# Performance work log

Hardware: AMD Instinct MI355X
Metric: run time of the kernel (lower is better)

The kernel has to match this reference:

```python
import jax, jax.numpy as jnp
import numpy as np

B, T, D, H = 4, 2048, 1024, 16
DH = D // H  # 64
EPS = 1e-5


def _layernorm(x, g, b):
    mu = jnp.mean(x, axis=-1, keepdims=True)
    var = jnp.var(x, axis=-1, keepdims=True)
    return (x - mu) * jax.lax.rsqrt(var + EPS) * g + b


def setup_inputs() -> dict:
    key = jax.random.key(0)
    ks = jax.random.split(key, 12)
    s = 0.02
    x = jax.random.normal(ks[0], (B, T, D), dtype=jnp.float32)
    # causal mask (the repo registers tril as the eos_mask buffer)
    eos_mask = jnp.broadcast_to(jnp.tril(jnp.ones((T, T), dtype=jnp.int32)), (B, T, T))
    Wq = jax.random.normal(ks[1], (H, D, DH), dtype=jnp.float32) * s
    Wk = jax.random.normal(ks[2], (H, D, DH), dtype=jnp.float32) * s
    Wv = jax.random.normal(ks[3], (H, D, DH), dtype=jnp.float32) * s
    Wp = jax.random.normal(ks[4], (D, D), dtype=jnp.float32) * s
    bp = jnp.zeros((D,), dtype=jnp.float32)
    W1 = jax.random.normal(ks[5], (D, 4 * D), dtype=jnp.float32) * s
    b1 = jnp.zeros((4 * D,), dtype=jnp.float32)
    W2 = jax.random.normal(ks[6], (4 * D, D), dtype=jnp.float32) * s
    b2 = jnp.zeros((D,), dtype=jnp.float32)
    g1 = jnp.ones((D,), dtype=jnp.float32)
    beta1 = jnp.zeros((D,), dtype=jnp.float32)
    g2 = jnp.ones((D,), dtype=jnp.float32)
    beta2 = jnp.zeros((D,), dtype=jnp.float32)
    return dict(x=x, eos_mask=eos_mask, Wq=Wq, Wk=Wk, Wv=Wv, Wp=Wp, bp=bp,
                W1=W1, b1=b1, W2=W2, b2=b2, g1=g1, beta1=beta1, g2=g2, beta2=beta2)


def reference(x, eos_mask, Wq, Wk, Wv, Wp, bp, W1, b1, W2, b2, g1, beta1, g2, beta2):
    # x: [B,T,D]; eos_mask: [B,T,T]
    x1 = _layernorm(x, g1, beta1)
    q = jnp.einsum('btd,hdk->bhtk', x1, Wq)
    k = jnp.einsum('btd,hdk->bhtk', x1, Wk)
    v = jnp.einsum('btd,hdk->bhtk', x1, Wv)
    # NOTE: original scales by 1/sqrt(C) where C = d_model (not d_head)
    scores = jnp.einsum('bhtk,bhsk->bhts', q, k) / np.sqrt(x.shape[-1]).astype(np.float32)
    scores = jnp.where(eos_mask[:, None, :, :] == 0, jnp.float32(-jnp.inf), scores)
    wei = jax.nn.softmax(scores, axis=-1)
    attn = jnp.einsum('bhts,bhsk->bhtk', wei, v)          # [B,H,T,DH]
    attn = attn.transpose(0, 2, 1, 3).reshape(x.shape)    # concat heads -> [B,T,D]
    attn = attn @ Wp + bp
    x2 = x1 + attn
    x3 = _layernorm(x2, g2, beta2)
    mlp = jax.nn.relu(x3 @ W1 + b1) @ W2 + b2
    out = x3 + mlp
    return out
```

## Files before the change

kernel.cpp:

```cpp
#include <hip/hip_runtime.h>


#define B_ 4
#define T_ 2048
#define D_ 1024
#define H_ 16
#define DH_ 64

using u16 = unsigned short;
typedef short bf16x8 __attribute__((ext_vector_type(8)));
typedef float f32x4 __attribute__((ext_vector_type(4)));

#define GLOAD_LDS16(g, l)                                                          \
  __builtin_amdgcn_global_load_lds((const __attribute__((address_space(1))) void*)(g), \
                                   (__attribute__((address_space(3))) void*)(l), 16, 0, 0)

#define CVTPK(d, lo, hi) asm("v_cvt_pk_bf16_f32 %0, %1, %2" : "=v"(d) : "v"(lo), "v"(hi))
#define BARSB() do { __builtin_amdgcn_s_barrier(); __builtin_amdgcn_sched_barrier(0); } while (0)

__device__ __forceinline__ f32x4 mfma16(bf16x8 a, bf16x8 b, f32x4 c) {
  return __builtin_amdgcn_mfma_f32_16x16x32_bf16(a, b, c, 0, 0, 0);
}

__device__ __forceinline__ u16 f2bf(float f) {
  union { float f; unsigned u; } v; v.f = f;
  unsigned r = v.u + 0x7fffu + ((v.u >> 16) & 1u);
  return (u16)(r >> 16);
}
__device__ __forceinline__ float bf2f(u16 h) {
  union { unsigned u; float f; } v; v.u = ((unsigned)h) << 16; return v.f;
}

template<typename TI>
__global__ __launch_bounds__(256)
void ln_kernel(const TI* __restrict__ x, const float* __restrict__ g,
               const float* __restrict__ be, u16* __restrict__ yb)
{
  const int row = blockIdx.x;
  const int tid = threadIdx.x;
  float v0, v1, v2, v3;
  if constexpr (sizeof(TI) == 4) {
    const float4 vx = ((const float4*)(x + (size_t)row * D_))[tid];
    v0 = vx.x; v1 = vx.y; v2 = vx.z; v3 = vx.w;
  } else {
    const ushort4 vx = ((const ushort4*)((const u16*)x + (size_t)row * D_))[tid];
    v0 = bf2f(vx.x); v1 = bf2f(vx.y); v2 = bf2f(vx.z); v3 = bf2f(vx.w);
  }
  float s  = v0 + v1 + v2 + v3;
  float s2 = v0*v0 + v1*v1 + v2*v2 + v3*v3;
#pragma unroll
  for (int m = 1; m < 64; m <<= 1) { s += __shfl_xor(s, m); s2 += __shfl_xor(s2, m); }
  __shared__ float red[8];
  const int w = tid >> 6;
  if ((tid & 63) == 0) { red[w] = s; red[4 + w] = s2; }
  __syncthreads();
  s  = red[0] + red[1] + red[2] + red[3];
  s2 = red[4] + red[5] + red[6] + red[7];
  const float mu   = s * (1.0f / D_);
  const float rstd = rsqrtf(s2 * (1.0f / D_) - mu * mu + 1e-5f);
  const float4 gg = ((const float4*)g)[tid];
  const float4 bb = ((const float4*)be)[tid];
  ushort4 pk;
  pk.x = f2bf((v0 - mu) * rstd * gg.x + bb.x);
  pk.y = f2bf((v1 - mu) * rstd * gg.y + bb.y);
  pk.z = f2bf((v2 - mu) * rstd * gg.z + bb.z);
  pk.w = f2bf((v3 - mu) * rstd * gg.w + bb.w);
  ((ushort4*)(yb + (size_t)row * D_))[tid] = pk;
}

__global__ __launch_bounds__(256)
void transpose_cvt(const float* __restrict__ in, u16* __restrict__ out, int R, int C)
{
  __shared__ float tile[32][33];
  const int c0 = blockIdx.x * 32, r0 = blockIdx.y * 32;
  const float* ip = in + (size_t)blockIdx.z * R * C;
  u16* op = out + (size_t)blockIdx.z * R * C;
  const int tx = threadIdx.x, ty = threadIdx.y;
#pragma unroll
  for (int j = 0; j < 4; ++j)
    tile[ty + j * 8][tx] = ip[(size_t)(r0 + ty + j * 8) * C + (c0 + tx)];
  __syncthreads();
#pragma unroll
  for (int j = 0; j < 4; ++j)
    op[(size_t)(c0 + ty + j * 8) * R + (r0 + tx)] = f2bf(tile[tx][ty + j * 8]);
}

__global__ __launch_bounds__(256)
void transpose_bf(const u16* __restrict__ in, u16* __restrict__ out, int R, int C)
{
  __shared__ u16 tile[32][34];
  const int c0 = blockIdx.x * 32, r0 = blockIdx.y * 32;
  const u16* ip = in + (size_t)blockIdx.z * R * C;
  u16* op = out + (size_t)blockIdx.z * R * C;
  const int tx = threadIdx.x, ty = threadIdx.y;
#pragma unroll
  for (int j = 0; j < 4; ++j)
    tile[ty + j * 8][tx] = ip[(size_t)(r0 + ty + j * 8) * C + (c0 + tx)];
  __syncthreads();
#pragma unroll
  for (int j = 0; j < 4; ++j)
    op[(size_t)(c0 + ty + j * 8) * R + (r0 + tx)] = tile[tx][ty + j * 8];
}

#define MODE_QKV 0
#define MODE_WP 1
#define MODE_MLP1 2
#define MODE_MLP2 3

template<int MODE>
__global__ __launch_bounds__(512, 2)
void gemm256v2(const u16* __restrict__ A, const u16* __restrict__ Bt,
               int M, int N, int K,
               const float* __restrict__ bias, const u16* __restrict__ resid,
               float* __restrict__ outf, u16* __restrict__ outb,
               u16* __restrict__ qo, u16* __restrict__ ko, u16* __restrict__ vo)
{
  __shared__ __align__(16) u16 Ash[2][256 * 64];
  __shared__ __align__(16) u16 Bsh[2][256 * 64];
  const int t = threadIdx.x, w = t >> 6, l = t & 63, lg = l >> 4, lr = l & 15;
  const int wr = w >> 2, wc = w & 3;

  const int gx = gridDim.x;
  const int nwg = gx * gridDim.y;
  const int bid = blockIdx.y * gx + blockIdx.x;
  const int cpx = nwg >> 3;
  const int virt = (bid & 7) * cpx + (bid >> 3);
  const int bn0 = (virt % gx) * 256, bm0 = (virt / gx) * 256;

  f32x4 acc[8][4] = {};

  const int srow = t >> 3;
  const int sc16 = (t & 7) ^ (srow & 7);
  const u16* gAs = A  + (size_t)(bm0 + srow) * K + sc16 * 8;
  const u16* gBs = Bt + (size_t)(bn0 + srow) * K + sc16 * 8;

#define ISS2_A(R, BUF, ko) GLOAD_LDS16(gAs + (size_t)(R) * 64 * K + (ko), &Ash[BUF][(R) * 4096 + w * 512])
#define ISS2_B(R, BUF, ko) GLOAD_LDS16(gBs + (size_t)(R) * 64 * K + (ko), &Bsh[BUF][(R) * 4096 + w * 512])

  const int nkt = K >> 6;
  ISS2_A(0, 0, 0); ISS2_A(1, 0, 0); ISS2_A(2, 0, 0); ISS2_A(3, 0, 0);
  ISS2_B(0, 0, 0); ISS2_B(1, 0, 0); ISS2_B(2, 0, 0); ISS2_B(3, 0, 0);
  if (nkt > 1) {
    ISS2_A(0, 1, 64); ISS2_A(1, 1, 64);
    asm volatile("s_waitcnt vmcnt(2)" ::: "memory");
  } else {
    asm volatile("s_waitcnt vmcnt(0)" ::: "memory");
  }
  BARSB();

  auto rdA = [&](int buf, int m) -> bf16x8 {
    const int r = wr * 128 + m * 16 + lr;
    return *(const bf16x8*)((const char*)&Ash[buf][0] + r * 128 + (((0 + lg) ^ (r & 7)) << 4));
  };
  auto rdA1 = [&](int buf, int m) -> bf16x8 {
    const int r = wr * 128 + m * 16 + lr;
    return *(const bf16x8*)((const char*)&Ash[buf][0] + r * 128 + (((4 + lg) ^ (r & 7)) << 4));
  };
  auto rdB0 = [&](int buf, int n) -> bf16x8 {
    const int r = wc * 64 + n * 16 + lr;
    return *(const bf16x8*)((const char*)&Bsh[buf][0] + r * 128 + (((0 + lg) ^ (r & 7)) << 4));
  };
  auto rdB1 = [&](int buf, int n) -> bf16x8 {
    const int r = wc * 64 + n * 16 + lr;
    return *(const bf16x8*)((const char*)&Bsh[buf][0] + r * 128 + (((4 + lg) ^ (r & 7)) << 4));
  };

  bf16x8 afr[4][2], bfr[4][2];

  for (int i = 0; i < nkt; ++i) {
    const int buf = i & 1, nb = buf ^ 1;
    const size_t k1 = (size_t)(i + 1) << 6, k2 = (size_t)(i + 2) << 6;
    const bool n1 = (i + 1 < nkt), n2 = (i + 2 < nkt);

#pragma unroll
    for (int m = 0; m < 4; ++m) { afr[m][0] = rdA(buf, m); afr[m][1] = rdA1(buf, m); }
#pragma unroll
    for (int n = 0; n < 2; ++n) { bfr[n][0] = rdB0(buf, n); bfr[n][1] = rdB1(buf, n); }
    if (n1) { ISS2_A(2, nb, k1); ISS2_A(3, nb, k1); }
    BARSB();
    __builtin_amdgcn_s_setprio(1);
#pragma unroll
    for (int m = 0; m < 4; ++m)
#pragma unroll
      for (int n = 0; n < 2; ++n) {
        acc[m][n] = mfma16(afr[m][0], bfr[n][0], acc[m][n]);
        acc[m][n] = mfma16(afr[m][1], bfr[n][1], acc[m][n]);
      }
    __builtin_amdgcn_s_setprio(0);
    BARSB();

#pragma unroll
    for (int n = 2; n < 4; ++n) { bfr[n][0] = rdB0(buf, n); bfr[n][1] = rdB1(buf, n); }
    if (n1) { ISS2_B(0, nb, k1); ISS2_B(1, nb, k1); }
    BARSB();
    __builtin_amdgcn_s_setprio(1);
#pragma unroll
    for (int m = 0; m < 4; ++m)
#pragma unroll
      for (int n = 2; n < 4; ++n) {
        acc[m][n] = mfma16(afr[m][0], bfr[n][0], acc[m][n]);
        acc[m][n] = mfma16(afr[m][1], bfr[n][1], acc[m][n]);
      }
    __builtin_amdgcn_s_setprio(0);
    BARSB();

#pragma unroll
    for (int m = 0; m < 4; ++m) { afr[m][0] = rdA(buf, 4 + m); afr[m][1] = rdA1(buf, 4 + m); }
    if (n1) { ISS2_B(2, nb, k1); ISS2_B(3, nb, k1); }
    BARSB();
    __builtin_amdgcn_s_setprio(1);
#pragma unroll
    for (int m = 0; m < 4; ++m)
#pragma unroll
      for (int n = 0; n < 2; ++n) {
        acc[4 + m][n] = mfma16(afr[m][0], bfr[n][0], acc[4 + m][n]);
        acc[4 + m][n] = mfma16(afr[m][1], bfr[n][1], acc[4 + m][n]);
      }
    __builtin_amdgcn_s_setprio(0);
    BARSB();

    if (n2) { ISS2_A(0, buf, k2); ISS2_A(1, buf, k2); }
    BARSB();
    __builtin_amdgcn_s_setprio(1);
#pragma unroll
    for (int m = 0; m < 4; ++m)
#pragma unroll
      for (int n = 2; n < 4; ++n) {
        acc[4 + m][n] = mfma16(afr[m][0], bfr[n][0], acc[4 + m][n]);
        acc[4 + m][n] = mfma16(afr[m][1], bfr[n][1], acc[4 + m][n]);
      }
    __builtin_amdgcn_s_setprio(0);
    if (n2) asm volatile("s_waitcnt vmcnt(2)" ::: "memory");
    else    asm volatile("s_waitcnt vmcnt(0)" ::: "memory");
    BARSB();
  }
#undef ISS2_A
#undef ISS2_B

#pragma unroll
  for (int m = 0; m < 8; ++m) {
#pragma unroll
    for (int n = 0; n < 4; ++n) {
#pragma unroll
      for (int r = 0; r < 4; ++r) {
        const int row = bm0 + wr * 128 + m * 16 + lg * 4 + r;
        const int col = bn0 + wc * 64 + n * 16 + lr;
        float v = acc[m][n][r];
        if constexpr (MODE == MODE_QKV) {
          const int sel = col >> 10, hh = (col >> 6) & 15, dh = col & 63;
          const int bi = row >> 11, tt = row & 2047;
          u16* dst = (sel == 0) ? qo : (sel == 1) ? ko : vo;
          dst[(((size_t)bi * H_ + hh) * T_ + tt) * DH_ + dh] = f2bf(v);
        } else if constexpr (MODE == MODE_MLP1) {
          v += bias[col];
          outb[(size_t)row * N + col] = f2bf(v > 0.f ? v : 0.f);
        }
      }
    }
  }
}

template<int MODE>
__global__ __launch_bounds__(512, 4)
void gemm128(const u16* __restrict__ A, const u16* __restrict__ Bt,
             int M, int N, int K,
             const float* __restrict__ bias, const u16* __restrict__ resid,
             float* __restrict__ outf, u16* __restrict__ outb,
             u16* __restrict__ qo, u16* __restrict__ ko, u16* __restrict__ vo)
{
  __shared__ __align__(16) u16 Ash[2][128 * 64];
  __shared__ __align__(16) u16 Bsh[2][128 * 64];
  const int t = threadIdx.x, w = t >> 6, l = t & 63, lg = l >> 4, lr = l & 15;
  const int wr = w >> 2, wc = w & 3;

  const int gx = gridDim.x;
  const int nwg = gx * gridDim.y;
  const int bid = blockIdx.y * gx + blockIdx.x;
  const int cpx = nwg >> 3;
  const int virt = (bid & 7) * cpx + (bid >> 3);
  const int bn0 = (virt % gx) * 128, bm0 = (virt / gx) * 128;

  f32x4 acc[4][2] = {};

  const int srow = t >> 3;
  const int sc16 = (t & 7) ^ (srow & 7);
  const u16* gAs = A  + (size_t)(bm0 + srow) * K + sc16 * 8;
  const u16* gBs = Bt + (size_t)(bn0 + srow) * K + sc16 * 8;

#define ISS_A(R, BUF, ko) GLOAD_LDS16(gAs + (size_t)(R) * 64 * K + (ko), &Ash[BUF][(R) * 4096 + w * 512])
#define ISS_B(R, BUF, ko) GLOAD_LDS16(gBs + (size_t)(R) * 64 * K + (ko), &Bsh[BUF][(R) * 4096 + w * 512])

  ISS_A(0, 0, 0); ISS_A(1, 0, 0); ISS_B(0, 0, 0); ISS_B(1, 0, 0);
  ISS_A(0, 1, 64); ISS_A(1, 1, 64); ISS_B(0, 1, 64); ISS_B(1, 1, 64);

  auto rdA = [&](int buf, int m, int kk) -> bf16x8 {
    const int r = wr * 64 + m * 16 + lr;
    return *(const bf16x8*)((const char*)&Ash[buf][0] + r * 128 + (((kk * 4 + lg) ^ (r & 7)) << 4));
  };
  auto rdB = [&](int buf, int n, int kk) -> bf16x8 {
    const int r = wc * 32 + n * 16 + lr;
    return *(const bf16x8*)((const char*)&Bsh[buf][0] + r * 128 + (((kk * 4 + lg) ^ (r & 7)) << 4));
  };

  const int nkt = K >> 6;
  for (int i = 0; i < nkt; ++i) {
    const int buf = i & 1;
    if (i + 1 < nkt) asm volatile("s_waitcnt vmcnt(4)" ::: "memory");
    else             asm volatile("s_waitcnt vmcnt(0)" ::: "memory");
    BARSB();

    bf16x8 afr[4][2], bfr[2][2];
#pragma unroll
    for (int m = 0; m < 4; ++m) { afr[m][0] = rdA(buf, m, 0); afr[m][1] = rdA(buf, m, 1); }
#pragma unroll
    for (int n = 0; n < 2; ++n) { bfr[n][0] = rdB(buf, n, 0); bfr[n][1] = rdB(buf, n, 1); }

    __builtin_amdgcn_s_setprio(1);
#pragma unroll
    for (int m = 0; m < 4; ++m)
#pragma unroll
      for (int n = 0; n < 2; ++n) {
        acc[m][n] = mfma16(afr[m][0], bfr[n][0], acc[m][n]);
        acc[m][n] = mfma16(afr[m][1], bfr[n][1], acc[m][n]);
      }
    __builtin_amdgcn_s_setprio(0);
    BARSB();

    if (i + 2 < nkt) {
      const size_t ko = (size_t)(i + 2) << 6;
      ISS_A(0, buf, ko); ISS_A(1, buf, ko); ISS_B(0, buf, ko); ISS_B(1, buf, ko);
    }
  }
#undef ISS_A
#undef ISS_B

#pragma unroll
  for (int m = 0; m < 4; ++m) {
#pragma unroll
    for (int n = 0; n < 2; ++n) {
#pragma unroll
      for (int r = 0; r < 4; ++r) {
        const int row = bm0 + wr * 64 + m * 16 + lg * 4 + r;
        const int col = bn0 + wc * 32 + n * 16 + lr;
        float v = acc[m][n][r];
        if constexpr (MODE == MODE_WP) {
          v += bias[col] + bf2f(resid[(size_t)row * N + col]);
          outb[(size_t)row * N + col] = f2bf(v);
        } else if constexpr (MODE == MODE_MLP2) {
          outf[(size_t)row * N + col] = v + bias[col] + bf2f(resid[(size_t)row * N + col]);
        }
      }
    }
  }
}

__global__ __launch_bounds__(256, 2)
void attn_kernel(const u16* __restrict__ q, const u16* __restrict__ k,
                 const u16* __restrict__ vt, u16* __restrict__ out)
{
  __shared__ __align__(16) u16 Ks[2][4096];
  __shared__ __align__(16) u16 Vs[2][4096];
  const int t = threadIdx.x, w = t >> 6, l = t & 63, lg = l >> 4, lr = l & 15;

  const int bid = blockIdx.x;
  const int virt = (bid & 7) * 256 + (bid >> 3);
  const int bh = (virt >> 8) * 8 + (virt & 7);
  const int qt = 31 - ((virt >> 3) & 31);

  const int b = bh >> 4, h = bh & 15;
  const u16* Qp  = q  + (size_t)bh * T_ * DH_;
  const u16* Kp  = k  + (size_t)bh * T_ * DH_;
  const u16* Vtp = vt + (size_t)bh * T_ * DH_;

  const int qrow = qt * 64 + w * 16 + lr;
  const bf16x8 qf0 = *(const bf16x8*)&Qp[(size_t)qrow * DH_ + lg * 8];
  const bf16x8 qf1 = *(const bf16x8*)&Qp[(size_t)qrow * DH_ + 32 + lg * 8];

  const int srow = t >> 3;
  const int schunk = ((t & 7) ^ (srow & 7)) << 3;
  const u16* Kg = Kp  + (size_t)srow * DH_ + schunk;
  const u16* Vg = Vtp + (size_t)srow * T_  + schunk;

  float m_run = -1e30f, l_run = 0.f;
  f32x4 o[4] = {};
  const float SC2 = 0.03125f * 1.44269504f;
  const float THR2 = 11.5416f;

  GLOAD_LDS16(Kg,            &Ks[0][w * 512]);
  GLOAD_LDS16(Kg + 32 * DH_, &Ks[0][2048 + w * 512]);
  GLOAD_LDS16(Vg,            &Vs[0][w * 512]);
  GLOAD_LDS16(Vg + 32 * T_,  &Vs[0][2048 + w * 512]);
  __syncthreads();

  const int nst = qt + 1;
  for (int st = 0; st < nst; ++st) {
    const int cur = st & 1, nxt = cur ^ 1;
    const bool pf = (st + 1 < nst);
    if (pf) {
      const u16* kg = Kg + (size_t)(st + 1) * 64 * DH_;
      const u16* vg = Vg + (size_t)(st + 1) * 64;
      GLOAD_LDS16(kg,            &Ks[nxt][w * 512]);
      GLOAD_LDS16(kg + 32 * DH_, &Ks[nxt][2048 + w * 512]);
      GLOAD_LDS16(vg,            &Vs[nxt][w * 512]);
      GLOAD_LDS16(vg + 32 * T_,  &Vs[nxt][2048 + w * 512]);
    }

    f32x4 sa[4] = {};
    const char* kb = (const char*)&Ks[cur][0];
    __builtin_amdgcn_s_setprio(1);
#pragma unroll
    for (int n = 0; n < 4; ++n) {
      const int sr = n * 16 + lr;
      const int base = (sr << 7) + (lg << 4);
      const int swz = (sr & 7) << 4;
      const bf16x8 b0 = *(const bf16x8*)(kb + (base ^ swz));
      const bf16x8 b1 = *(const bf16x8*)(kb + ((base + 64) ^ swz));
      sa[n] = mfma16(b0, qf0, sa[n]);
      sa[n] = mfma16(b1, qf1, sa[n]);
    }
    __builtin_amdgcn_s_setprio(0);

    float sc[4][4];
    float rm = -1e30f;
#pragma unroll
    for (int n = 0; n < 4; ++n)
#pragma unroll
      for (int r = 0; r < 4; ++r) {
        float x = sa[n][r] * SC2;
        if (st == qt && (st * 64 + n * 16 + lg * 4 + r) > qrow) x = -1e30f;
        sc[n][r] = x;
        rm = fmaxf(rm, x);
      }
    rm = fmaxf(rm, __shfl_xor(rm, 16));
    rm = fmaxf(rm, __shfl_xor(rm, 32));
    const bool noresc = __all(rm <= m_run + THR2);
    if (!noresc) {
      const float mnew = fmaxf(m_run, rm);
      const float al = exp2f(m_run - mnew);
      m_run = mnew;
      l_run *= al;
      const float alr0 = __shfl(al, lg * 4 + 0);
      const float alr1 = __shfl(al, lg * 4 + 1);
      const float alr2 = __shfl(al, lg * 4 + 2);
      const float alr3 = __shfl(al, lg * 4 + 3);
#pragma unroll
      for (int n = 0; n < 4; ++n) {
        o[n][0] *= alr0; o[n][1] *= alr1; o[n][2] *= alr2; o[n][3] *= alr3;
      }
    }
    float p[4][4];
    float rs = 0.f;
#pragma unroll
    for (int n = 0; n < 4; ++n)
#pragma unroll
      for (int r = 0; r < 4; ++r) {
        p[n][r] = exp2f(sc[n][r] - m_run);
        rs += p[n][r];
      }
    rs += __shfl_xor(rs, 16);
    rs += __shfl_xor(rs, 32);
    l_run += rs;

    unsigned pk0a, pk0b, pk1a, pk1b, pk2a, pk2b, pk3a, pk3b;
    CVTPK(pk0a, p[0][0], p[0][1]); CVTPK(pk0b, p[0][2], p[0][3]);
    CVTPK(pk1a, p[1][0], p[1][1]); CVTPK(pk1b, p[1][2], p[1][3]);
    CVTPK(pk2a, p[2][0], p[2][1]); CVTPK(pk2b, p[2][2], p[2][3]);
    CVTPK(pk3a, p[3][0], p[3][1]); CVTPK(pk3b, p[3][2], p[3][3]);

    const int srcA = lr + ((l >> 4) & 1) * 32;
    const int srcB = srcA + 16;
    const bool hi = (l >> 5) & 1;
    union { uint4 u; bf16x8 v8; } f0, f1;
    {
      const unsigned xA0 = __shfl(pk0a, srcA), xA1 = __shfl(pk0b, srcA);
      const unsigned yA0 = __shfl(pk1a, srcA), yA1 = __shfl(pk1b, srcA);
      const unsigned xB0 = __shfl(pk0a, srcB), xB1 = __shfl(pk0b, srcB);
      const unsigned yB0 = __shfl(pk1a, srcB), yB1 = __shfl(pk1b, srcB);
      f0.u.x = hi ? yA0 : xA0; f0.u.y = hi ? yA1 : xA1;
      f0.u.z = hi ? yB0 : xB0; f0.u.w = hi ? yB1 : xB1;
    }
    {
      const unsigned xA0 = __shfl(pk2a, srcA), xA1 = __shfl(pk2b, srcA);
      const unsigned yA0 = __shfl(pk3a, srcA), yA1 = __shfl(pk3b, srcA);
      const unsigned xB0 = __shfl(pk2a, srcB), xB1 = __shfl(pk2b, srcB);
      const unsigned yB0 = __shfl(pk3a, srcB), yB1 = __shfl(pk3b, srcB);
      f1.u.x = hi ? yA0 : xA0; f1.u.y = hi ? yA1 : xA1;
      f1.u.z = hi ? yB0 : xB0; f1.u.w = hi ? yB1 : xB1;
    }

    const char* vbase = (const char*)&Vs[cur][0];
    __builtin_amdgcn_s_setprio(1);
#pragma unroll
    for (int ks = 0; ks < 2; ++ks) {
      const bf16x8 pa = ks ? f1.v8 : f0.v8;
#pragma unroll
      for (int n = 0; n < 4; ++n) {
        const int dh = n * 16 + lr;
        const int base = (dh << 7) + (ks << 6) + (lg << 4);
        const int swz = (dh & 7) << 4;
        const bf16x8 vbf = *(const bf16x8*)(vbase + (base ^ swz));
        o[n] = mfma16(pa, vbf, o[n]);
      }
    }
    __builtin_amdgcn_s_setprio(0);

    __syncthreads();
  }

  const size_t obase = ((size_t)b * T_) * D_ + (size_t)h * DH_;
  float li[4];
  li[0] = 1.0f / __shfl(l_run, lg * 4 + 0);
  li[1] = 1.0f / __shfl(l_run, lg * 4 + 1);
  li[2] = 1.0f / __shfl(l_run, lg * 4 + 2);
  li[3] = 1.0f / __shfl(l_run, lg * 4 + 3);
#pragma unroll
  for (int n = 0; n < 4; ++n) {
#pragma unroll
    for (int r = 0; r < 4; ++r) {
      const int qg = qt * 64 + w * 16 + lg * 4 + r;
      out[obase + (size_t)qg * D_ + n * 16 + lr] = f2bf(o[n][r] * li[r]);
    }
  }
}

extern "C" void kernel_launch(void* const* d_in, const int* in_sizes, int n_in,
                              void* d_out, int out_size, void* d_ws, size_t ws_size,
                              hipStream_t stream) {
  (void)in_sizes; (void)n_in; (void)out_size; (void)ws_size;
  const float* x   = (const float*)d_in[0];
  const float* Wq  = (const float*)d_in[2];
  const float* Wk  = (const float*)d_in[3];
  const float* Wv  = (const float*)d_in[4];
  const float* Wp  = (const float*)d_in[5];
  const float* bp  = (const float*)d_in[6];
  const float* W1  = (const float*)d_in[7];
  const float* b1  = (const float*)d_in[8];
  const float* W2  = (const float*)d_in[9];
  const float* b2  = (const float*)d_in[10];
  const float* g1  = (const float*)d_in[11];
  const float* be1 = (const float*)d_in[12];
  const float* g2  = (const float*)d_in[13];
  const float* be2 = (const float*)d_in[14];

  char* ws = (char*)d_ws;
  const size_t MB16 = 16777216;
  u16* x1b   = (u16*)(ws);
  u16* qb    = (u16*)(ws + 1 * MB16);
  u16* kb    = (u16*)(ws + 2 * MB16);
  u16* vb    = (u16*)(ws + 3 * MB16);
  u16* attnb = (u16*)(ws + 4 * MB16);
  u16* x2b   = (u16*)(ws + 5 * MB16);
  u16* hb    = (u16*)(ws + 6 * MB16);
  u16* vtb   = hb;
  u16* wqkvb = (u16*)(ws + 10 * MB16);
  u16* wpb   = (u16*)(ws + 10 * MB16 + 6291456);
  u16* w1b   = (u16*)(ws + 10 * MB16 + 8388608);
  u16* w2b   = (u16*)(ws + 11 * MB16);
  u16* x3b   = qb;

  dim3 tb(32, 8, 1);
  transpose_cvt<<<dim3(2, 32, 16),  tb, 0, stream>>>(Wq, wqkvb,                    1024, 64);
  transpose_cvt<<<dim3(2, 32, 16),  tb, 0, stream>>>(Wk, wqkvb + (size_t)1048576,  1024, 64);
  transpose_cvt<<<dim3(2, 32, 16),  tb, 0, stream>>>(Wv, wqkvb + (size_t)2097152,  1024, 64);
  transpose_cvt<<<dim3(32, 32, 1),  tb, 0, stream>>>(Wp, wpb, 1024, 1024);
  transpose_cvt<<<dim3(128, 32, 1), tb, 0, stream>>>(W1, w1b, 1024, 4096);
  transpose_cvt<<<dim3(32, 128, 1), tb, 0, stream>>>(W2, w2b, 4096, 1024);

  ln_kernel<float><<<8192, 256, 0, stream>>>(x, g1, be1, x1b);

  gemm256v2<MODE_QKV><<<dim3(12, 32), 512, 0, stream>>>(
      x1b, wqkvb, 8192, 3072, 1024, nullptr, nullptr, nullptr, nullptr, qb, kb, vb);

  transpose_bf<<<dim3(2, 64, 64), tb, 0, stream>>>(vb, vtb, 2048, 64);

  attn_kernel<<<dim3(2048), 256, 0, stream>>>(qb, kb, vtb, attnb);

  gemm128<MODE_WP><<<dim3(8, 64), 512, 0, stream>>>(
      attnb, wpb, 8192, 1024, 1024, bp, x1b, nullptr, x2b, nullptr, nullptr, nullptr);

  ln_kernel<u16><<<8192, 256, 0, stream>>>(x2b, g2, be2, x3b);

  gemm256v2<MODE_MLP1><<<dim3(16, 32), 512, 0, stream>>>(
      x3b, w1b, 8192, 4096, 1024, b1, nullptr, nullptr, hb, nullptr, nullptr, nullptr);

  gemm128<MODE_MLP2><<<dim3(8, 64), 512, 0, stream>>>(
      hb, w2b, 8192, 1024, 4096, b2, x3b, (float*)d_out, nullptr, nullptr, nullptr, nullptr);
}
```

Baseline: 375.0 us.

## Enlarge attention query tile to 128 rows with 8 waves per block

The attention kernel now runs 512 threads (8 waves) per block covering 128 query rows, so each K/V tile loaded into LDS is shared by twice as many waves. The grid is halved and the block-to-(batch, head, q-tile) mapping is rewritten to match. Each thread issues one global-to-LDS load per tile instead of two, and causal masking applies to the last two key tiles. This lowers K/V global traffic and load instructions per query row, at the cost of coarser causal work granularity, fewer blocks for load balance, and more waves contending for registers.

```diff
diff --git a/kernel.cpp b/kernel.cpp
--- a/kernel.cpp
+++ b/kernel.cpp
@@ -354,7 +354,7 @@
   }
 }
 
-__global__ __launch_bounds__(256, 2)
+__global__ __launch_bounds__(512, 4)
 void attn_kernel(const u16* __restrict__ q, const u16* __restrict__ k,
                  const u16* __restrict__ vt, u16* __restrict__ out)
 {
@@ -363,16 +363,16 @@
   const int t = threadIdx.x, w = t >> 6, l = t & 63, lg = l >> 4, lr = l & 15;
 
   const int bid = blockIdx.x;
-  const int virt = (bid & 7) * 256 + (bid >> 3);
-  const int bh = (virt >> 8) * 8 + (virt & 7);
-  const int qt = 31 - ((virt >> 3) & 31);
+  const int virt = (bid & 7) * 128 + (bid >> 3);
+  const int bh = (virt >> 7) * 8 + (virt & 7);
+  const int qt = 15 - ((virt >> 3) & 15);
 
   const int b = bh >> 4, h = bh & 15;
   const u16* Qp  = q  + (size_t)bh * T_ * DH_;
   const u16* Kp  = k  + (size_t)bh * T_ * DH_;
   const u16* Vtp = vt + (size_t)bh * T_ * DH_;
 
-  const int qrow = qt * 64 + w * 16 + lr;
+  const int qrow = qt * 128 + w * 16 + lr;
   const bf16x8 qf0 = *(const bf16x8*)&Qp[(size_t)qrow * DH_ + lg * 8];
   const bf16x8 qf1 = *(const bf16x8*)&Qp[(size_t)qrow * DH_ + 32 + lg * 8];
 
@@ -386,23 +386,17 @@
   const float SC2 = 0.03125f * 1.44269504f;
   const float THR2 = 11.5416f;
 
-  GLOAD_LDS16(Kg,            &Ks[0][w * 512]);
-  GLOAD_LDS16(Kg + 32 * DH_, &Ks[0][2048 + w * 512]);
-  GLOAD_LDS16(Vg,            &Vs[0][w * 512]);
-  GLOAD_LDS16(Vg + 32 * T_,  &Vs[0][2048 + w * 512]);
+  GLOAD_LDS16(Kg, &Ks[0][w * 512]);
+  GLOAD_LDS16(Vg, &Vs[0][w * 512]);
   __syncthreads();
 
-  const int nst = qt + 1;
+  const int nst = 2 * qt + 2;
   for (int st = 0; st < nst; ++st) {
     const int cur = st & 1, nxt = cur ^ 1;
     const bool pf = (st + 1 < nst);
     if (pf) {
-      const u16* kg = Kg + (size_t)(st + 1) * 64 * DH_;
-      const u16* vg = Vg + (size_t)(st + 1) * 64;
-      GLOAD_LDS16(kg,            &Ks[nxt][w * 512]);
-      GLOAD_LDS16(kg + 32 * DH_, &Ks[nxt][2048 + w * 512]);
-      GLOAD_LDS16(vg,            &Vs[nxt][w * 512]);
-      GLOAD_LDS16(vg + 32 * T_,  &Vs[nxt][2048 + w * 512]);
+      GLOAD_LDS16(Kg + (size_t)(st + 1) * 64 * DH_, &Ks[nxt][w * 512]);
+      GLOAD_LDS16(Vg + (size_t)(st + 1) * 64,       &Vs[nxt][w * 512]);
     }
 
     f32x4 sa[4] = {};
@@ -425,12 +419,20 @@
 #pragma unroll
     for (int n = 0; n < 4; ++n)
 #pragma unroll
-      for (int r = 0; r < 4; ++r) {
-        float x = sa[n][r] * SC2;
-        if (st == qt && (st * 64 + n * 16 + lg * 4 + r) > qrow) x = -1e30f;
-        sc[n][r] = x;
-        rm = fmaxf(rm, x);
-      }
+      for (int r = 0; r < 4; ++r)
+        sc[n][r] = sa[n][r] * SC2;
+    if (st >= 2 * qt) {
+#pragma unroll
+      for (int n = 0; n < 4; ++n)
+#pragma unroll
+        for (int r = 0; r < 4; ++r)
+          if (st * 64 + n * 16 + lg * 4 + r > qrow) sc[n][r] = -1e30f;
+    }
+#pragma unroll
+    for (int n = 0; n < 4; ++n)
+#pragma unroll
+      for (int r = 0; r < 4; ++r)
+        rm = fmaxf(rm, sc[n][r]);
     rm = fmaxf(rm, __shfl_xor(rm, 16));
     rm = fmaxf(rm, __shfl_xor(rm, 32));
     const bool noresc = __all(rm <= m_run + THR2);
@@ -448,24 +450,23 @@
         o[n][0] *= alr0; o[n][1] *= alr1; o[n][2] *= alr2; o[n][3] *= alr3;
       }
     }
-    float p[4][4];
     float rs = 0.f;
 #pragma unroll
     for (int n = 0; n < 4; ++n)
 #pragma unroll
       for (int r = 0; r < 4; ++r) {
-        p[n][r] = exp2f(sc[n][r] - m_run);
-        rs += p[n][r];
+        sc[n][r] = exp2f(sc[n][r] - m_run);
+        rs += sc[n][r];
       }
     rs += __shfl_xor(rs, 16);
     rs += __shfl_xor(rs, 32);
     l_run += rs;
 
     unsigned pk0a, pk0b, pk1a, pk1b, pk2a, pk2b, pk3a, pk3b;
-    CVTPK(pk0a, p[0][0], p[0][1]); CVTPK(pk0b, p[0][2], p[0][3]);
-    CVTPK(pk1a, p[1][0], p[1][1]); CVTPK(pk1b, p[1][2], p[1][3]);
-    CVTPK(pk2a, p[2][0], p[2][1]); CVTPK(pk2b, p[2][2], p[2][3]);
-    CVTPK(pk3a, p[3][0], p[3][1]); CVTPK(pk3b, p[3][2], p[3][3]);
+    CVTPK(pk0a, sc[0][0], sc[0][1]); CVTPK(pk0b, sc[0][2], sc[0][3]);
+    CVTPK(pk1a, sc[1][0], sc[1][1]); CVTPK(pk1b, sc[1][2], sc[1][3]);
+    CVTPK(pk2a, sc[2][0], sc[2][1]); CVTPK(pk2b, sc[2][2], sc[2][3]);
+    CVTPK(pk3a, sc[3][0], sc[3][1]); CVTPK(pk3b, sc[3][2], sc[3][3]);
 
     const int srcA = lr + ((l >> 4) & 1) * 32;
     const int srcB = srcA + 16;
@@ -517,7 +518,7 @@
   for (int n = 0; n < 4; ++n) {
 #pragma unroll
     for (int r = 0; r < 4; ++r) {
-      const int qg = qt * 64 + w * 16 + lg * 4 + r;
+      const int qg = qt * 128 + w * 16 + lg * 4 + r;
       out[obase + (size_t)qg * D_ + n * 16 + lr] = f2bf(o[n][r] * li[r]);
     }
   }
@@ -573,7 +574,7 @@
 
   transpose_bf<<<dim3(2, 64, 64), tb, 0, stream>>>(vb, vtb, 2048, 64);
 
-  attn_kernel<<<dim3(2048), 256, 0, stream>>>(qb, kb, vtb, attnb);
+  attn_kernel<<<dim3(1024), 512, 0, stream>>>(qb, kb, vtb, attnb);
 
   gemm128<MODE_WP><<<dim3(8, 64), 512, 0, stream>>>(
       attnb, wpb, 8192, 1024, 1024, bp, x1b, nullptr, x2b, nullptr, nullptr, nullptr);
```

Measured after the change: 365.9 us. 2.4% less time.
